# Optimization experiments

Hardware: AMD Instinct MI355X
Metric: run time of the kernel (lower is better)

## Reference

```python
import jax, jax.numpy as jnp
import numpy as np

N_NODES = 10000
N_EDGES = 320000
K_HOPS = 3
IN_CH = 128
OUT_CH = 128


def setup_inputs() -> dict:
    key = jax.random.key(0)
    k1, k2, k3, k4, k5 = jax.random.split(key, 5)
    h = jax.random.normal(k1, (N_NODES, IN_CH), dtype=jnp.float32)
    X = jax.random.normal(k2, (N_EDGES, K_HOPS), dtype=jnp.float32)
    edge_index = jax.random.randint(k3, (2, N_EDGES), 0, N_NODES, dtype=jnp.int64)
    batch_node = jax.random.uniform(k4, (N_NODES,), dtype=jnp.float32)
    # glorot init for weight, zeros for bias (matches reset_parameters)
    stdv = np.sqrt(6.0 / (IN_CH + OUT_CH))
    weight = jax.random.uniform(k5, (K_HOPS, IN_CH, OUT_CH), dtype=jnp.float32,
                                minval=-stdv, maxval=stdv)
    bias = jnp.zeros((OUT_CH,), dtype=jnp.float32)
    return {"h": h, "X": X, "edge_index": edge_index,
            "batch_node": batch_node, "weight": weight, "bias": bias}


def reference(h, X, edge_index, batch_node, weight, bias):
    # Original builds dense A[k, src, dst] = X[e, k] (zeros elsewhere), then
    # res = A @ h @ weight, max over k, + bias. We honor the sparsity:
    # agg[src, k, :] = sum_e X[e, k] * h[dst[e], :]  (sparse A @ h per hop k)
    n = batch_node.shape[0]
    src = edge_index[0]
    dst = edge_index[1]
    msg = X[:, :, None] * h[dst][:, None, :]                 # [E, K, in]
    agg = jax.ops.segment_sum(msg, src, num_segments=n)      # [N, K, in]
    res = jnp.einsum('nki,kio->kno', agg, weight)            # [K, N, out]
    out = res.max(axis=0) + bias                             # [N, out]
    return out
```

## Files before the change

### kernel.cpp

```cpp
#include <hip/hip_runtime.h>

#define N_NODES 10000
#define N_EDGES 320000
#define K_HOPS  3
#define CH      128
#define NBF     4
#define ROWP    136
#define SUBSLOT 44
#define SLOT    88
#define SEPAD   96
#define CSTRIDE 16

#define EDGE_BLKS 1250
#define HCV_BLKS  1250
#define WCV_BLKS  192

typedef __attribute__((ext_vector_type(8))) short  frag8;
typedef __attribute__((ext_vector_type(4))) float  floatx4;

__device__ inline unsigned short f2bf(float x) {
    union { float f; unsigned u; } v; v.f = x;
    unsigned r = v.u + 0x7fff + ((v.u >> 16) & 1);
    return (unsigned short)(r >> 16);
}

__global__ __launch_bounds__(256) void prep_fill_kernel(
    const float* __restrict__ h, const float* __restrict__ X,
    const int* __restrict__ ei, const float* __restrict__ W,
    unsigned short* __restrict__ hb, unsigned short* __restrict__ WT,
    int* __restrict__ cursor, uint2* __restrict__ edata)
{
    int b = blockIdx.x;
    if (b < EDGE_BLKS) {
        int e = b * 256 + threadIdx.x;
        int src = ei[e];
        int dst = ei[N_EDGES + e];
        int j = e & 1;
        int r = atomicAdd(cursor + (2 * src + j) * CSTRIDE, 1);
        if (r < SUBSLOT) {
            uint2 rec;
            rec.x = (unsigned)f2bf(X[e * K_HOPS + 0])
                  | ((unsigned)f2bf(X[e * K_HOPS + 1]) << 16);
            rec.y = (unsigned)f2bf(X[e * K_HOPS + 2])
                  | ((unsigned)dst << 16);
            edata[(size_t)src * SLOT + j * SUBSLOT + r] = rec;
        }
    } else if (b < EDGE_BLKS + HCV_BLKS) {
        int tid = (b - EDGE_BLKS) * 256 + threadIdx.x;
        float4 v = *(const float4*)(h + (size_t)tid * 4);
        ushort4 p;
        p.x = f2bf(v.x); p.y = f2bf(v.y); p.z = f2bf(v.z); p.w = f2bf(v.w);
        *(ushort4*)(hb + (size_t)tid * 4) = p;
    } else {
        int tid = (b - EDGE_BLKS - HCV_BLKS) * 256 + threadIdx.x;
        int i = tid & 127;
        int o = (tid >> 7) & 127;
        int k = tid >> 14;
        WT[tid] = f2bf(W[((size_t)k * CH + i) * CH + o]);
    }
}

__device__ inline void estep(uint2 er, uint2 q, float (&a)[12]) {
    float x0 = __uint_as_float(er.x << 16);
    float x1 = __uint_as_float(er.x & 0xffff0000u);
    float x2 = __uint_as_float(er.y << 16);
    float h0 = __uint_as_float(q.x << 16);
    float h1 = __uint_as_float(q.x & 0xffff0000u);
    float h2 = __uint_as_float(q.y << 16);
    float h3 = __uint_as_float(q.y & 0xffff0000u);
    a[0] = fmaf(x0, h0, a[0]); a[1]  = fmaf(x0, h1, a[1]);
    a[2] = fmaf(x0, h2, a[2]); a[3]  = fmaf(x0, h3, a[3]);
    a[4] = fmaf(x1, h0, a[4]); a[5]  = fmaf(x1, h1, a[5]);
    a[6] = fmaf(x1, h2, a[6]); a[7]  = fmaf(x1, h3, a[7]);
    a[8] = fmaf(x2, h0, a[8]); a[9]  = fmaf(x2, h1, a[9]);
    a[10]= fmaf(x2, h2, a[10]); a[11]= fmaf(x2, h3, a[11]);
}

__global__ __launch_bounds__(256) void fused_kernel(
    const unsigned short* __restrict__ hb,
    const uint2*          __restrict__ edata,
    const int*            __restrict__ cursor,
    const unsigned short* __restrict__ WT,
    const float*          __restrict__ bias,
    float*                __restrict__ out)
{
    __shared__ unsigned short sA[K_HOPS][16][ROWP];
    __shared__ uint2 sE[NBF][SEPAD];
    const int node0 = blockIdx.x * NBF;
    const int t    = threadIdx.x;
    const int w    = t >> 6;
    const int lane = t & 63;
    const int half = lane >> 5;
    const int cq   = (lane & 31) * 4;

    const int n = node0 + w;
    int c0 = __builtin_amdgcn_readfirstlane(min(cursor[(2 * n + 0) * CSTRIDE], SUBSLOT));
    int c1 = __builtin_amdgcn_readfirstlane(min(cursor[(2 * n + 1) * CSTRIDE], SUBSLOT));
    const int cnt = c0 + c1;
    const uint2* ebase = edata + (size_t)n * SLOT;

    if (lane < c0) sE[w][lane] = ebase[lane];
    if (lane < c1) sE[w][c0 + lane] = ebase[SUBSLOT + lane];
    {
        int z0 = cnt + lane, z1 = cnt + 64 + lane;
        uint2 zz; zz.x = 0u; zz.y = 0u;
        if (z0 < SEPAD) sE[w][z0] = zz;
        if (z1 < SEPAD) sE[w][z1] = zz;
    }

    float acc[12];
#pragma unroll
    for (int i = 0; i < 12; ++i) acc[i] = 0.f;

    const int groups = (cnt + 15) >> 4;
    for (int g = 0; g < groups; ++g) {
        const int s = g * 8;
        uint2 er[8], q[8];
#pragma unroll
        for (int k = 0; k < 8; ++k) er[k] = sE[w][2 * (s + k) + half];
#pragma unroll
        for (int k = 0; k < 8; ++k)
            q[k] = *(const uint2*)(hb + ((size_t)(er[k].y >> 16) << 7) + cq);
#pragma unroll
        for (int k = 0; k < 8; ++k) estep(er[k], q[k], acc);
    }

#pragma unroll
    for (int i = 0; i < 12; ++i) acc[i] += __shfl_xor(acc[i], 32, 64);

    if (half == 0) {
#pragma unroll
        for (int hop = 0; hop < K_HOPS; ++hop) {
            ushort4 p;
            p.x = f2bf(acc[4 * hop + 0]); p.y = f2bf(acc[4 * hop + 1]);
            p.z = f2bf(acc[4 * hop + 2]); p.w = f2bf(acc[4 * hop + 3]);
            *(ushort4*)&sA[hop][w][cq] = p;
        }
    }
    __syncthreads();

    const int col  = lane & 15;
    const int quad = lane >> 4;
    const int ob   = 32 * w;

    floatx4 m0 = {-3.4e38f, -3.4e38f, -3.4e38f, -3.4e38f};
    floatx4 m1 = m0;
#pragma unroll
    for (int hop = 0; hop < K_HOPS; ++hop) {
        floatx4 c0v = {0.f, 0.f, 0.f, 0.f};
        floatx4 c1v = {0.f, 0.f, 0.f, 0.f};
        const unsigned short* arow = &sA[hop][col][quad * 8];
        const unsigned short* b0p  = WT + ((size_t)hop * CH + ob + col) * CH + quad * 8;
        const unsigned short* b1p  = b0p + 16 * CH;
#pragma unroll
        for (int kt = 0; kt < 4; ++kt) {
            frag8 af  = *(const frag8*)(arow + kt * 32);
            frag8 bf0 = *(const frag8*)(b0p + kt * 32);
            frag8 bf1 = *(const frag8*)(b1p + kt * 32);
            c0v = __builtin_amdgcn_mfma_f32_16x16x32_bf16(af, bf0, c0v, 0, 0, 0);
            c1v = __builtin_amdgcn_mfma_f32_16x16x32_bf16(af, bf1, c1v, 0, 0, 0);
        }
#pragma unroll
        for (int r = 0; r < 4; ++r) {
            m0[r] = fmaxf(m0[r], c0v[r]);
            m1[r] = fmaxf(m1[r], c1v[r]);
        }
    }

    if (quad == 0) {
        const float bv0 = bias[ob + col];
        const float bv1 = bias[ob + 16 + col];
#pragma unroll
        for (int r = 0; r < 4; ++r) {
            out[(size_t)(node0 + r) * CH + ob + col]      = m0[r] + bv0;
            out[(size_t)(node0 + r) * CH + ob + 16 + col] = m1[r] + bv1;
        }
    }
}

extern "C" void kernel_launch(void* const* d_in, const int* in_sizes, int n_in,
                              void* d_out, int out_size, void* d_ws, size_t ws_size,
                              hipStream_t stream) {
    const float* h    = (const float*)d_in[0];
    const float* X    = (const float*)d_in[1];
    const int*   ei   = (const int*)  d_in[2];
    const float* W    = (const float*)d_in[4];
    const float* bias = (const float*)d_in[5];
    float*       out  = (float*)d_out;

    char* ws = (char*)d_ws;
    int* cursor = (int*)ws;                        ws += (size_t)N_NODES * 2 * CSTRIDE * sizeof(int);
    unsigned short* hb = (unsigned short*)ws;      ws += (size_t)N_NODES * CH * sizeof(unsigned short);
    unsigned short* WT = (unsigned short*)ws;      ws += (size_t)K_HOPS * CH * CH * sizeof(unsigned short);
    uint2* edata = (uint2*)ws;

    hipMemsetAsync(cursor, 0, (size_t)N_NODES * 2 * CSTRIDE * sizeof(int), stream);

    prep_fill_kernel<<<EDGE_BLKS + HCV_BLKS + WCV_BLKS, 256, 0, stream>>>(
        h, X, ei, W, hb, WT, cursor, edata);
    fused_kernel<<<N_NODES / NBF, 256, 0, stream>>>(hb, edata, cursor, WT, bias, out);
}
```

Measured before the change: 125.5 us.

## Process 16 nodes per block with two nodes per wave, full MFMA tile

Each block now handles 16 nodes with 8 waves, and each wave gathers two nodes' edge lists at once. This gives more independent loads in flight, and the 16-row MFMA A tile is now fully used instead of only 4 of 16 rows. Each wave computes one 16-column output slice, so the WT fragments each block loads are shared across four times as many nodes. The cost is more registers per wave, a gather loop bounded by the larger of the two nodes' edge counts, and fewer, larger blocks.

New measurement: 111.0 us. -11.6%, faster.

```diff
diff --git a/kernel.cpp b/kernel.cpp
--- a/kernel.cpp
+++ b/kernel.cpp
@@ -4,7 +4,7 @@
 #define N_EDGES 320000
 #define K_HOPS  3
 #define CH      128
-#define NBF     4
+#define NBF     16
 #define ROWP    136
 #define SUBSLOT 44
 #define SLOT    88
@@ -76,7 +76,7 @@
     a[10]= fmaf(x2, h2, a[10]); a[11]= fmaf(x2, h3, a[11]);
 }
 
-__global__ __launch_bounds__(256) void fused_kernel(
+__global__ __launch_bounds__(512) void fused_kernel(
     const unsigned short* __restrict__ hb,
     const uint2*          __restrict__ edata,
     const int*            __restrict__ cursor,
@@ -93,88 +93,99 @@
     const int half = lane >> 5;
     const int cq   = (lane & 31) * 4;
 
-    const int n = node0 + w;
-    int c0 = __builtin_amdgcn_readfirstlane(min(cursor[(2 * n + 0) * CSTRIDE], SUBSLOT));
-    int c1 = __builtin_amdgcn_readfirstlane(min(cursor[(2 * n + 1) * CSTRIDE], SUBSLOT));
-    const int cnt = c0 + c1;
-    const uint2* ebase = edata + (size_t)n * SLOT;
-
-    if (lane < c0) sE[w][lane] = ebase[lane];
-    if (lane < c1) sE[w][c0 + lane] = ebase[SUBSLOT + lane];
+    const int rA = 2 * w, rB = rA + 1;
+    const int nA = node0 + rA, nB = node0 + rB;
+    int a0 = __builtin_amdgcn_readfirstlane(min(cursor[(2 * nA + 0) * CSTRIDE], SUBSLOT));
+    int a1 = __builtin_amdgcn_readfirstlane(min(cursor[(2 * nA + 1) * CSTRIDE], SUBSLOT));
+    int b0 = __builtin_amdgcn_readfirstlane(min(cursor[(2 * nB + 0) * CSTRIDE], SUBSLOT));
+    int b1 = __builtin_amdgcn_readfirstlane(min(cursor[(2 * nB + 1) * CSTRIDE], SUBSLOT));
+    const int cA = a0 + a1, cB = b0 + b1;
+    const uint2* eA = edata + (size_t)nA * SLOT;
+    const uint2* eB = edata + (size_t)nB * SLOT;
+
+    if (lane < a0) sE[rA][lane]      = eA[lane];
+    if (lane < a1) sE[rA][a0 + lane] = eA[SUBSLOT + lane];
+    if (lane < b0) sE[rB][lane]      = eB[lane];
+    if (lane < b1) sE[rB][b0 + lane] = eB[SUBSLOT + lane];
     {
-        int z0 = cnt + lane, z1 = cnt + 64 + lane;
         uint2 zz; zz.x = 0u; zz.y = 0u;
-        if (z0 < SEPAD) sE[w][z0] = zz;
-        if (z1 < SEPAD) sE[w][z1] = zz;
-    }
-
-    float acc[12];
-#pragma unroll
-    for (int i = 0; i < 12; ++i) acc[i] = 0.f;
-
-    const int groups = (cnt + 15) >> 4;
-    for (int g = 0; g < groups; ++g) {
+        int zA0 = cA + lane, zA1 = cA + 64 + lane;
+        if (zA0 < SEPAD) sE[rA][zA0] = zz;
+        if (zA1 < SEPAD) sE[rA][zA1] = zz;
+        int zB0 = cB + lane, zB1 = cB + 64 + lane;
+        if (zB0 < SEPAD) sE[rB][zB0] = zz;
+        if (zB1 < SEPAD) sE[rB][zB1] = zz;
+    }
+
+    float accA[12], accB[12];
+#pragma unroll
+    for (int i = 0; i < 12; ++i) { accA[i] = 0.f; accB[i] = 0.f; }
+
+    const int gmax = (max(cA, cB) + 15) >> 4;
+    for (int g = 0; g < gmax; ++g) {
         const int s = g * 8;
-        uint2 er[8], q[8];
-#pragma unroll
-        for (int k = 0; k < 8; ++k) er[k] = sE[w][2 * (s + k) + half];
+        uint2 erA[8], erB[8], qA[8], qB[8];
+#pragma unroll
+        for (int k = 0; k < 8; ++k) erA[k] = sE[rA][2 * (s + k) + half];
+#pragma unroll
+        for (int k = 0; k < 8; ++k) erB[k] = sE[rB][2 * (s + k) + half];
 #pragma unroll
         for (int k = 0; k < 8; ++k)
-            q[k] = *(const uint2*)(hb + ((size_t)(er[k].y >> 16) << 7) + cq);
-#pragma unroll
-        for (int k = 0; k < 8; ++k) estep(er[k], q[k], acc);
-    }
-
-#pragma unroll
-    for (int i = 0; i < 12; ++i) acc[i] += __shfl_xor(acc[i], 32, 64);
+            qA[k] = *(const uint2*)(hb + ((size_t)(erA[k].y >> 16) << 7) + cq);
+#pragma unroll
+        for (int k = 0; k < 8; ++k)
+            qB[k] = *(const uint2*)(hb + ((size_t)(erB[k].y >> 16) << 7) + cq);
+#pragma unroll
+        for (int k = 0; k < 8; ++k) estep(erA[k], qA[k], accA);
+#pragma unroll
+        for (int k = 0; k < 8; ++k) estep(erB[k], qB[k], accB);
+    }
+
+#pragma unroll
+    for (int i = 0; i < 12; ++i) {
+        accA[i] += __shfl_xor(accA[i], 32, 64);
+        accB[i] += __shfl_xor(accB[i], 32, 64);
+    }
 
     if (half == 0) {
 #pragma unroll
         for (int hop = 0; hop < K_HOPS; ++hop) {
-            ushort4 p;
-            p.x = f2bf(acc[4 * hop + 0]); p.y = f2bf(acc[4 * hop + 1]);
-            p.z = f2bf(acc[4 * hop + 2]); p.w = f2bf(acc[4 * hop + 3]);
-            *(ushort4*)&sA[hop][w][cq] = p;
+            ushort4 pA, pB;
+            pA.x = f2bf(accA[4 * hop + 0]); pA.y = f2bf(accA[4 * hop + 1]);
+            pA.z = f2bf(accA[4 * hop + 2]); pA.w = f2bf(accA[4 * hop + 3]);
+            pB.x = f2bf(accB[4 * hop + 0]); pB.y = f2bf(accB[4 * hop + 1]);
+            pB.z = f2bf(accB[4 * hop + 2]); pB.w = f2bf(accB[4 * hop + 3]);
+            *(ushort4*)&sA[hop][rA][cq] = pA;
+            *(ushort4*)&sA[hop][rB][cq] = pB;
         }
     }
     __syncthreads();
 
     const int col  = lane & 15;
     const int quad = lane >> 4;
-    const int ob   = 32 * w;
+    const int ob   = 16 * w;
 
     floatx4 m0 = {-3.4e38f, -3.4e38f, -3.4e38f, -3.4e38f};
-    floatx4 m1 = m0;
 #pragma unroll
     for (int hop = 0; hop < K_HOPS; ++hop) {
-        floatx4 c0v = {0.f, 0.f, 0.f, 0.f};
-        floatx4 c1v = {0.f, 0.f, 0.f, 0.f};
+        floatx4 cv = {0.f, 0.f, 0.f, 0.f};
         const unsigned short* arow = &sA[hop][col][quad * 8];
-        const unsigned short* b0p  = WT + ((size_t)hop * CH + ob + col) * CH + quad * 8;
-        const unsigned short* b1p  = b0p + 16 * CH;
+        const unsigned short* bp   = WT + ((size_t)hop * CH + ob + col) * CH + quad * 8;
 #pragma unroll
         for (int kt = 0; kt < 4; ++kt) {
-            frag8 af  = *(const frag8*)(arow + kt * 32);
-            frag8 bf0 = *(const frag8*)(b0p + kt * 32);
-            frag8 bf1 = *(const frag8*)(b1p + kt * 32);
-            c0v = __builtin_amdgcn_mfma_f32_16x16x32_bf16(af, bf0, c0v, 0, 0, 0);
-            c1v = __builtin_amdgcn_mfma_f32_16x16x32_bf16(af, bf1, c1v, 0, 0, 0);
+            frag8 af = *(const frag8*)(arow + kt * 32);
+            frag8 bf = *(const frag8*)(bp + kt * 32);
+            cv = __builtin_amdgcn_mfma_f32_16x16x32_bf16(af, bf, cv, 0, 0, 0);
         }
 #pragma unroll
-        for (int r = 0; r < 4; ++r) {
-            m0[r] = fmaxf(m0[r], c0v[r]);
-            m1[r] = fmaxf(m1[r], c1v[r]);
-        }
-    }
-
-    if (quad == 0) {
-        const float bv0 = bias[ob + col];
-        const float bv1 = bias[ob + 16 + col];
-#pragma unroll
-        for (int r = 0; r < 4; ++r) {
-            out[(size_t)(node0 + r) * CH + ob + col]      = m0[r] + bv0;
-            out[(size_t)(node0 + r) * CH + ob + 16 + col] = m1[r] + bv1;
-        }
+        for (int r = 0; r < 4; ++r) m0[r] = fmaxf(m0[r], cv[r]);
+    }
+
+    const float bv = bias[ob + col];
+#pragma unroll
+    for (int r = 0; r < 4; ++r) {
+        int row = quad * 4 + r;
+        out[(size_t)(node0 + row) * CH + ob + col] = m0[r] + bv;
     }
 }
 
@@ -198,5 +209,6 @@
 
     prep_fill_kernel<<<EDGE_BLKS + HCV_BLKS + WCV_BLKS, 256, 0, stream>>>(
         h, X, ei, W, hb, WT, cursor, edata);
-    fused_kernel<<<N_NODES / NBF, 256, 0, stream>>>(hb, edata, cursor, WT, bias, out);
-}
+    fused_kernel<<<(N_NODES + NBF - 1) / NBF, 512, 0, stream>>>(
+        hb, edata, cursor, WT, bias, out);
+}
```
